# Kernel optimization log

Measured on AMD Instinct MI355X. Metric: run time of the kernel, lower is better.

The kernel has to match this reference:

```python
import jax, jax.numpy as jnp
import numpy as np

B, S, E, H = 2, 2048, 1024, 16
D = E // H  # head_dim = 64


def setup_inputs() -> dict:
    key = jax.random.key(0)
    ks = jax.random.split(key, 6)
    sc = 1.0 / np.sqrt(D)
    return {
        "x": jax.random.normal(ks[0], (B, S, E), dtype=jnp.float32),
        "Wq": jax.random.normal(ks[1], (D, D), dtype=jnp.float32) * sc,
        "Wk": jax.random.normal(ks[2], (D, D), dtype=jnp.float32) * sc,
        "Wv": jax.random.normal(ks[3], (D, D), dtype=jnp.float32) * sc,
        "Wo": jax.random.normal(ks[4], (E, E), dtype=jnp.float32) * (1.0 / np.sqrt(E)),
        "bo": jnp.zeros((E,), dtype=jnp.float32),
    }


def reference(x, Wq, Wk, Wv, Wo, bo):
    b, s, e = x.shape
    # split into heads: (B, H, S, D)
    xh = x.reshape(b, s, H, D).transpose(0, 2, 1, 3)
    # per-head linear projections (weights SHARED across heads); torch Linear: x @ W^T
    q = jnp.einsum('bhsd,ed->bhse', xh, Wq)
    k = jnp.einsum('bhsd,ed->bhse', xh, Wk)
    v = jnp.einsum('bhsd,ed->bhse', xh, Wv)
    # full attention matrix (B, H, S, S) — faithful to the naive original
    energy = jnp.einsum('bhqd,bhkd->bhqk', q, k)
    attn = jax.nn.softmax(energy / jnp.sqrt(jnp.asarray(D, x.dtype)), axis=-1)
    out = jnp.einsum('bhqk,bhkd->bhqd', attn, v)
    out = out.transpose(0, 2, 1, 3).reshape(b, s, e)
    return out @ Wo.T + bo
```

## Files before the change

kernel.cpp:

```cpp
#include <hip/hip_runtime.h>
#include <hip/hip_bf16.h>

#define B 2
#define S 2048
#define E 1024
#define H 16
#define D 64

typedef unsigned short ushort_t;
typedef __attribute__((ext_vector_type(8))) short bf16x8;
typedef __attribute__((ext_vector_type(4))) float f32x4;
typedef __attribute__((ext_vector_type(16))) float f32x16;

static __device__ __forceinline__ ushort_t f2bf(float f) {
    union { float f; unsigned u; } v; v.f = f;
    unsigned r = v.u + 0x7fffu + ((v.u >> 16) & 1u);
    return (ushort_t)(r >> 16);
}

#define MFMA(a, b, c)   __builtin_amdgcn_mfma_f32_16x16x32_bf16((a), (b), (c), 0, 0, 0)
#define MFMA32(a, b, c) __builtin_amdgcn_mfma_f32_32x32x16_bf16((a), (b), (c), 0, 0, 0)
#define PACKBF(hi, lo) __builtin_amdgcn_perm((hi), (lo), 0x07060302u)

__global__ __launch_bounds__(256) void cvt_w(
    const float* __restrict__ Wq, const float* __restrict__ Wk, const float* __restrict__ Wv,
    const float* __restrict__ Wo,
    ushort_t* __restrict__ wqb, ushort_t* __restrict__ wkb, ushort_t* __restrict__ wvb,
    ushort_t* __restrict__ wob)
{
    int gid = blockIdx.x, t = threadIdx.x;
    if (gid < 1024) {
        int i = gid * 1024 + t * 4;
        float4 f = *(const float4*)(Wo + i);
        ushort4 u; u.x = f2bf(f.x); u.y = f2bf(f.y); u.z = f2bf(f.z); u.w = f2bf(f.w);
        *(ushort4*)(wob + i) = u;
    } else {
        int idx = (gid - 1024) * 1024 + t * 4;
        int which = idx >> 12, off = idx & 4095;
        const float* src = (which == 0) ? Wq : (which == 1) ? Wk : Wv;
        ushort_t* dst    = (which == 0) ? wqb : (which == 1) ? wkb : wvb;
        float sc = (which == 0) ? 0.18033688011112042f : 1.0f;
        float4 f = *(const float4*)(src + off);
        ushort4 u; u.x = f2bf(f.x * sc); u.y = f2bf(f.y * sc);
        u.z = f2bf(f.z * sc); u.w = f2bf(f.w * sc);
        *(ushort4*)(dst + off) = u;
    }
}

__global__ __launch_bounds__(256) void qkv_proj(
    const float* __restrict__ x,
    const ushort_t* __restrict__ wq, const ushort_t* __restrict__ wk, const ushort_t* __restrict__ wv,
    ushort_t* __restrict__ q, ushort_t* __restrict__ k, ushort_t* __restrict__ vT)
{
    __shared__ ushort_t Xs[64][72];
    __shared__ ushort_t Wqs[64][72], Wks[64][72], Wvs[64][72];
    int t = threadIdx.x;
    int bh = blockIdx.y, b = bh >> 4, h = bh & 15;
    int s0 = blockIdx.x * 64;

    {
        int i = t >> 2, d0 = (t & 3) * 16;
        const float* xp = x + ((size_t)(b * S + s0 + i)) * E + h * D + d0;
        #pragma unroll
        for (int c = 0; c < 16; c += 4) {
            float4 f = *(const float4*)(xp + c);
            Xs[i][d0 + c + 0] = f2bf(f.x); Xs[i][d0 + c + 1] = f2bf(f.y);
            Xs[i][d0 + c + 2] = f2bf(f.z); Xs[i][d0 + c + 3] = f2bf(f.w);
        }
    }
    {
        int e = t >> 2, d0 = (t & 3) * 16;
        *(bf16x8*)&Wqs[e][d0]     = *(const bf16x8*)(wq + e * 64 + d0);
        *(bf16x8*)&Wqs[e][d0 + 8] = *(const bf16x8*)(wq + e * 64 + d0 + 8);
        *(bf16x8*)&Wks[e][d0]     = *(const bf16x8*)(wk + e * 64 + d0);
        *(bf16x8*)&Wks[e][d0 + 8] = *(const bf16x8*)(wk + e * 64 + d0 + 8);
        *(bf16x8*)&Wvs[e][d0]     = *(const bf16x8*)(wv + e * 64 + d0);
        *(bf16x8*)&Wvs[e][d0 + 8] = *(const bf16x8*)(wv + e * 64 + d0 + 8);
    }
    __syncthreads();

    int w = t >> 6, lane = t & 63, m = lane & 15, quad = lane >> 4;
    bf16x8 a0 = *(bf16x8*)&Xs[16 * w + m][quad * 8];
    bf16x8 a1 = *(bf16x8*)&Xs[16 * w + m][32 + quad * 8];
    f32x4 cq[4], ck[4], cv[4];
    #pragma unroll
    for (int nt = 0; nt < 4; nt++) { cq[nt] = (f32x4)0.f; ck[nt] = (f32x4)0.f; cv[nt] = (f32x4)0.f; }
    #pragma unroll
    for (int nt = 0; nt < 4; nt++) {
        bf16x8 b0, b1;
        b0 = *(bf16x8*)&Wqs[nt * 16 + m][quad * 8]; b1 = *(bf16x8*)&Wqs[nt * 16 + m][32 + quad * 8];
        cq[nt] = MFMA(a0, b0, cq[nt]); cq[nt] = MFMA(a1, b1, cq[nt]);
        b0 = *(bf16x8*)&Wks[nt * 16 + m][quad * 8]; b1 = *(bf16x8*)&Wks[nt * 16 + m][32 + quad * 8];
        ck[nt] = MFMA(a0, b0, ck[nt]); ck[nt] = MFMA(a1, b1, ck[nt]);
        b0 = *(bf16x8*)&Wvs[nt * 16 + m][quad * 8]; b1 = *(bf16x8*)&Wvs[nt * 16 + m][32 + quad * 8];
        cv[nt] = MFMA(a0, b0, cv[nt]); cv[nt] = MFMA(a1, b1, cv[nt]);
    }
    size_t base = (size_t)bh * S + s0;
    #pragma unroll
    for (int nt = 0; nt < 4; nt++)
        #pragma unroll
        for (int r = 0; r < 4; r++) {
            size_t idx = (base + 16 * w + quad * 4 + r) * D + nt * 16 + m;
            q[idx] = f2bf(cq[nt][r]);
            k[idx] = f2bf(ck[nt][r]);
        }
    __syncthreads();
    #pragma unroll
    for (int nt = 0; nt < 4; nt++)
        #pragma unroll
        for (int r = 0; r < 4; r++)
            Wvs[nt * 16 + m][16 * w + quad * 4 + r] = f2bf(cv[nt][r]);
    __syncthreads();
    {
        int d0 = t >> 2, sc = (t & 3) * 16;
        ushort_t* vp = vT + ((size_t)bh * D + d0) * S + s0 + sc;
        *(bf16x8*)(vp)     = *(bf16x8*)&Wvs[d0][sc];
        *(bf16x8*)(vp + 8) = *(bf16x8*)&Wvs[d0][sc + 8];
    }
}

__global__ __launch_bounds__(512, 4) void flash_attn(
    const ushort_t* __restrict__ q, const ushort_t* __restrict__ k,
    const ushort_t* __restrict__ vT, ushort_t* __restrict__ ao)
{
    __shared__ ushort_t Ks[2][2][64][72];
    __shared__ ushort_t Vt[2][2][64][72];
    int t = threadIdx.x;
    int bh = blockIdx.y, b = bh >> 4, h = bh & 15;
    int q0 = blockIdx.x * 128;
    int w = t >> 6, lane = t & 63, l31 = lane & 31, half = lane >> 5;
    int g = w >> 2, wq = w & 3;
    int tg = t & 255;

    const ushort_t* qb = q + ((size_t)bh * S + q0) * D;
    const ushort_t* kb = k + (size_t)bh * S * D;
    const ushort_t* vb = vT + (size_t)bh * D * S;

    bf16x8 qf[4];
    {
        const ushort_t* qp = qb + (size_t)(wq * 32 + l31) * D + half * 8;
        #pragma unroll
        for (int c = 0; c < 4; c++) qf[c] = *(const bf16x8*)(qp + c * 16);
    }

    f32x16 o0 = (f32x16)0.f, o1 = (f32x16)0.f;
    float2 ls2 = make_float2(0.f, 0.f);

    int sr = tg >> 2, scc = (tg & 3) * 16;
    bf16x8 kp0, kp1, vp0, vp1;

    {
        int k00 = g * 64;
        const ushort_t* kp = kb + (size_t)(k00 + sr) * D + scc;
        const ushort_t* vp = vb + (size_t)sr * S + k00 + scc;
        kp0 = *(const bf16x8*)(kp);     kp1 = *(const bf16x8*)(kp + 8);
        vp0 = *(const bf16x8*)(vp);     vp1 = *(const bf16x8*)(vp + 8);
        *(bf16x8*)&Ks[g][0][sr][scc]     = kp0;
        *(bf16x8*)&Ks[g][0][sr][scc + 8] = kp1;
        *(bf16x8*)&Vt[g][0][sr][scc]     = vp0;
        *(bf16x8*)&Vt[g][0][sr][scc + 8] = vp1;
    }
    __syncthreads();
    {
        int k01 = (2 + g) * 64;
        const ushort_t* kp = kb + (size_t)(k01 + sr) * D + scc;
        const ushort_t* vp = vb + (size_t)sr * S + k01 + scc;
        kp0 = *(const bf16x8*)(kp);     kp1 = *(const bf16x8*)(kp + 8);
        vp0 = *(const bf16x8*)(vp);     vp1 = *(const bf16x8*)(vp + 8);
    }

    const int NJ = S / 128;
    for (int jt = 0; jt < NJ; jt++) {
        int p = jt & 1;
        if (jt + 1 < NJ) {
            *(bf16x8*)&Ks[g][1 - p][sr][scc]     = kp0;
            *(bf16x8*)&Ks[g][1 - p][sr][scc + 8] = kp1;
            *(bf16x8*)&Vt[g][1 - p][sr][scc]     = vp0;
            *(bf16x8*)&Vt[g][1 - p][sr][scc + 8] = vp1;
        }
        if (jt + 2 < NJ) {
            int k0n = (2 * (jt + 2) + g) * 64;
            const ushort_t* kp = kb + (size_t)(k0n + sr) * D + scc;
            const ushort_t* vp = vb + (size_t)sr * S + k0n + scc;
            kp0 = *(const bf16x8*)(kp);     kp1 = *(const bf16x8*)(kp + 8);
            vp0 = *(const bf16x8*)(vp);     vp1 = *(const bf16x8*)(vp + 8);
        }

        union { unsigned u[4]; bf16x8 v; } pa[4];
        #pragma unroll
        for (int st = 0; st < 2; st++) {
            f32x16 e = (f32x16)0.f;
            #pragma unroll
            for (int c = 0; c < 4; c++) {
                bf16x8 ka = *(bf16x8*)&Ks[g][p][st * 32 + l31][c * 16 + half * 8];
                e = MFMA32(ka, qf[c], e);
            }
            unsigned pt[16];
            #pragma unroll
            for (int r = 0; r < 16; r += 2) {
                float pe0 = __builtin_amdgcn_exp2f(e[r]);
                float pe1 = __builtin_amdgcn_exp2f(e[r + 1]);
                ls2.x += pe0; ls2.y += pe1;
                pt[r]     = __float_as_uint(pe0);
                pt[r + 1] = __float_as_uint(pe1);
            }
            #pragma unroll
            for (int c2 = 0; c2 < 2; c2++) {
                int rb = c2 * 8;
                unsigned dA = PACKBF(pt[rb + 1], pt[rb + 0]);
                unsigned dB = PACKBF(pt[rb + 3], pt[rb + 2]);
                unsigned dC = PACKBF(pt[rb + 5], pt[rb + 4]);
                unsigned dD = PACKBF(pt[rb + 7], pt[rb + 6]);
                unsigned x1 = (unsigned)__shfl_xor((int)(half ? dA : dC), 32, 64);
                unsigned x2 = (unsigned)__shfl_xor((int)(half ? dB : dD), 32, 64);
                int kc = st * 2 + c2;
                pa[kc].u[0] = half ? x1 : dA;
                pa[kc].u[1] = half ? x2 : dB;
                pa[kc].u[2] = half ? dC : x1;
                pa[kc].u[3] = half ? dD : x2;
            }
        }

        #pragma unroll
        for (int kc = 0; kc < 4; kc++) {
            bf16x8 vf0 = *(bf16x8*)&Vt[g][p][l31][kc * 16 + half * 8];
            bf16x8 vf1 = *(bf16x8*)&Vt[g][p][32 + l31][kc * 16 + half * 8];
            o0 = MFMA32(pa[kc].v, vf0, o0);
            o1 = MFMA32(pa[kc].v, vf1, o1);
        }
        __syncthreads();
    }

    float lsum = ls2.x + ls2.y;
    float* cmb = (float*)&Ks[0][0][0][0];
    int slot = (wq * 64 + lane) * 33;
    if (g == 1) {
        #pragma unroll
        for (int r2 = 0; r2 < 16; r2++) { cmb[slot + r2] = o0[r2]; cmb[slot + 16 + r2] = o1[r2]; }
        cmb[slot + 32] = lsum;
    }
    __syncthreads();
    if (g == 0) {
        #pragma unroll
        for (int r2 = 0; r2 < 16; r2++) { o0[r2] += cmb[slot + r2]; o1[r2] += cmb[slot + 16 + r2]; }
        lsum += cmb[slot + 32];
        float lfull = lsum + __shfl_xor(lsum, 32, 64);
        float inv = 1.001953125f / lfull;
        #pragma unroll
        for (int reg = 0; reg < 16; reg++) {
            int qrow = (reg & 3) + 8 * (reg >> 2) + 4 * half;
            float li = __shfl(inv, qrow, 64);
            int srow = q0 + wq * 32 + qrow;
            size_t base2 = ((size_t)(b * S + srow)) * E + h * D + l31;
            ao[base2]      = f2bf(o0[reg] * li);
            ao[base2 + 32] = f2bf(o1[reg] * li);
        }
    }
}

__global__ __launch_bounds__(256) void out_proj(
    const ushort_t* __restrict__ A, const ushort_t* __restrict__ Wob,
    const float* __restrict__ bo, float* __restrict__ Y)
{
    __shared__ ushort_t As[2][128][72];
    __shared__ ushort_t Ws[2][64][72];
    int t = threadIdx.x;
    int n0 = blockIdx.x * 64, m0 = blockIdx.y * 128;
    int w = t >> 6, lane = t & 63, m = lane & 15, quad = lane >> 4;
    f32x4 acc[2][4];
    #pragma unroll
    for (int u = 0; u < 2; u++)
        #pragma unroll
        for (int nt = 0; nt < 4; nt++) acc[u][nt] = (f32x4)0.f;

    int ar = t >> 1, ac = (t & 1) * 32;
    int wr = t >> 2, wc = (t & 3) * 16;
    const ushort_t* apb = A + (size_t)(m0 + ar) * E + ac;
    const ushort_t* wpb = Wob + (size_t)(n0 + wr) * E + wc;

    bf16x8 arg[4], wrg[2];
    {
        #pragma unroll
        for (int i = 0; i < 4; i++) *(bf16x8*)&As[0][ar][ac + 8 * i] = *(const bf16x8*)(apb + 8 * i);
        *(bf16x8*)&Ws[0][wr][wc]     = *(const bf16x8*)(wpb);
        *(bf16x8*)&Ws[0][wr][wc + 8] = *(const bf16x8*)(wpb + 8);
    }
    __syncthreads();
    {
        #pragma unroll
        for (int i = 0; i < 4; i++) arg[i] = *(const bf16x8*)(apb + 64 + 8 * i);
        wrg[0] = *(const bf16x8*)(wpb + 64);
        wrg[1] = *(const bf16x8*)(wpb + 64 + 8);
    }

    const int KT = E / 64;
    for (int ks = 0; ks < KT; ks++) {
        int p = ks & 1;
        if (ks + 1 < KT) {
            #pragma unroll
            for (int i = 0; i < 4; i++) *(bf16x8*)&As[1 - p][ar][ac + 8 * i] = arg[i];
            *(bf16x8*)&Ws[1 - p][wr][wc]     = wrg[0];
            *(bf16x8*)&Ws[1 - p][wr][wc + 8] = wrg[1];
        }
        if (ks + 2 < KT) {
            int off = (ks + 2) * 64;
            #pragma unroll
            for (int i = 0; i < 4; i++) arg[i] = *(const bf16x8*)(apb + off + 8 * i);
            wrg[0] = *(const bf16x8*)(wpb + off);
            wrg[1] = *(const bf16x8*)(wpb + off + 8);
        }
        #pragma unroll
        for (int h2 = 0; h2 < 2; h2++) {
            bf16x8 af[2];
            af[0] = *(bf16x8*)&As[p][w * 32 + m][h2 * 32 + quad * 8];
            af[1] = *(bf16x8*)&As[p][w * 32 + 16 + m][h2 * 32 + quad * 8];
            #pragma unroll
            for (int nt = 0; nt < 4; nt++) {
                bf16x8 bfr = *(bf16x8*)&Ws[p][nt * 16 + m][h2 * 32 + quad * 8];
                acc[0][nt] = MFMA(af[0], bfr, acc[0][nt]);
                acc[1][nt] = MFMA(af[1], bfr, acc[1][nt]);
            }
        }
        __syncthreads();
    }
    #pragma unroll
    for (int u = 0; u < 2; u++)
        #pragma unroll
        for (int nt = 0; nt < 4; nt++)
            #pragma unroll
            for (int r = 0; r < 4; r++) {
                int row = m0 + w * 32 + u * 16 + quad * 4 + r;
                int col = n0 + nt * 16 + m;
                Y[(size_t)row * E + col] = acc[u][nt][r] + bo[col];
            }
}

extern "C" void kernel_launch(void* const* d_in, const int* in_sizes, int n_in,
                              void* d_out, int out_size, void* d_ws, size_t ws_size,
                              hipStream_t stream)
{
    const float* x  = (const float*)d_in[0];
    const float* Wq = (const float*)d_in[1];
    const float* Wk = (const float*)d_in[2];
    const float* Wv = (const float*)d_in[3];
    const float* Wo = (const float*)d_in[4];
    const float* bo = (const float*)d_in[5];
    float* Y = (float*)d_out;

    const size_t n = (size_t)B * H * S * D;
    ushort_t* qw  = (ushort_t*)d_ws;
    ushort_t* kw  = qw + n;
    ushort_t* vTw = kw + n;
    ushort_t* ao  = vTw + n;
    ushort_t* wob = ao + n;
    ushort_t* wqb = wob + (size_t)E * E;
    ushort_t* wkb = wqb + D * D;
    ushort_t* wvb = wkb + D * D;

    cvt_w<<<dim3(1024 + 12), 256, 0, stream>>>(Wq, Wk, Wv, Wo, wqb, wkb, wvb, wob);
    qkv_proj<<<dim3(S / 64, B * H), 256, 0, stream>>>(x, wqb, wkb, wvb, qw, kw, vTw);
    flash_attn<<<dim3(S / 128, B * H), 512, 0, stream>>>(qw, kw, vTw, ao);
    out_proj<<<dim3(E / 64, (B * S) / 128), 256, 0, stream>>>(ao, wob, bo, Y);
}
```

Baseline: 146.7 us.

## Fuse weight conversion into QKV projection, use permlane32 swap, swizzle out_proj blocks

Removes the separate weight-conversion kernel. The Wo bf16 conversion now runs inside the qkv_proj grid, one 1024-element chunk per block, and each block converts the small Wq/Wk/Wv tiles straight into shared memory. In flash attention the cross-half shuffle plus selects is replaced with v_permlane32_swap_b32 inline asm. out_proj block indices are remapped with a swizzle meant to improve L2 reuse. The goal is to save one kernel launch and some shuffle overhead, at the cost of redundant per-block conversion of the small weights.

```diff
diff --git a/kernel.cpp b/kernel.cpp
--- a/kernel.cpp
+++ b/kernel.cpp
@@ -22,35 +22,12 @@
 #define MFMA32(a, b, c) __builtin_amdgcn_mfma_f32_32x32x16_bf16((a), (b), (c), 0, 0, 0)
 #define PACKBF(hi, lo) __builtin_amdgcn_perm((hi), (lo), 0x07060302u)
 
-__global__ __launch_bounds__(256) void cvt_w(
+__global__ __launch_bounds__(256) void qkv_proj(
+    const float* __restrict__ x,
     const float* __restrict__ Wq, const float* __restrict__ Wk, const float* __restrict__ Wv,
     const float* __restrict__ Wo,
-    ushort_t* __restrict__ wqb, ushort_t* __restrict__ wkb, ushort_t* __restrict__ wvb,
+    ushort_t* __restrict__ q, ushort_t* __restrict__ k, ushort_t* __restrict__ vT,
     ushort_t* __restrict__ wob)
-{
-    int gid = blockIdx.x, t = threadIdx.x;
-    if (gid < 1024) {
-        int i = gid * 1024 + t * 4;
-        float4 f = *(const float4*)(Wo + i);
-        ushort4 u; u.x = f2bf(f.x); u.y = f2bf(f.y); u.z = f2bf(f.z); u.w = f2bf(f.w);
-        *(ushort4*)(wob + i) = u;
-    } else {
-        int idx = (gid - 1024) * 1024 + t * 4;
-        int which = idx >> 12, off = idx & 4095;
-        const float* src = (which == 0) ? Wq : (which == 1) ? Wk : Wv;
-        ushort_t* dst    = (which == 0) ? wqb : (which == 1) ? wkb : wvb;
-        float sc = (which == 0) ? 0.18033688011112042f : 1.0f;
-        float4 f = *(const float4*)(src + off);
-        ushort4 u; u.x = f2bf(f.x * sc); u.y = f2bf(f.y * sc);
-        u.z = f2bf(f.z * sc); u.w = f2bf(f.w * sc);
-        *(ushort4*)(dst + off) = u;
-    }
-}
-
-__global__ __launch_bounds__(256) void qkv_proj(
-    const float* __restrict__ x,
-    const ushort_t* __restrict__ wq, const ushort_t* __restrict__ wk, const ushort_t* __restrict__ wv,
-    ushort_t* __restrict__ q, ushort_t* __restrict__ k, ushort_t* __restrict__ vT)
 {
     __shared__ ushort_t Xs[64][72];
     __shared__ ushort_t Wqs[64][72], Wks[64][72], Wvs[64][72];
@@ -59,6 +36,13 @@
     int s0 = blockIdx.x * 64;
 
     {
+        int woid = blockIdx.y * 32 + blockIdx.x;
+        int i = woid * 1024 + t * 4;
+        float4 f = *(const float4*)(Wo + i);
+        ushort4 u2; u2.x = f2bf(f.x); u2.y = f2bf(f.y); u2.z = f2bf(f.z); u2.w = f2bf(f.w);
+        *(ushort4*)(wob + i) = u2;
+    }
+    {
         int i = t >> 2, d0 = (t & 3) * 16;
         const float* xp = x + ((size_t)(b * S + s0 + i)) * E + h * D + d0;
         #pragma unroll
@@ -70,12 +54,23 @@
     }
     {
         int e = t >> 2, d0 = (t & 3) * 16;
-        *(bf16x8*)&Wqs[e][d0]     = *(const bf16x8*)(wq + e * 64 + d0);
-        *(bf16x8*)&Wqs[e][d0 + 8] = *(const bf16x8*)(wq + e * 64 + d0 + 8);
-        *(bf16x8*)&Wks[e][d0]     = *(const bf16x8*)(wk + e * 64 + d0);
-        *(bf16x8*)&Wks[e][d0 + 8] = *(const bf16x8*)(wk + e * 64 + d0 + 8);
-        *(bf16x8*)&Wvs[e][d0]     = *(const bf16x8*)(wv + e * 64 + d0);
-        *(bf16x8*)&Wvs[e][d0 + 8] = *(const bf16x8*)(wv + e * 64 + d0 + 8);
+        const float* wqp = Wq + e * 64 + d0;
+        const float* wkp = Wk + e * 64 + d0;
+        const float* wvp = Wv + e * 64 + d0;
+        #pragma unroll
+        for (int c = 0; c < 16; c += 4) {
+            float4 fq = *(const float4*)(wqp + c);
+            Wqs[e][d0 + c + 0] = f2bf(fq.x * 0.18033688011112042f);
+            Wqs[e][d0 + c + 1] = f2bf(fq.y * 0.18033688011112042f);
+            Wqs[e][d0 + c + 2] = f2bf(fq.z * 0.18033688011112042f);
+            Wqs[e][d0 + c + 3] = f2bf(fq.w * 0.18033688011112042f);
+            float4 fk = *(const float4*)(wkp + c);
+            Wks[e][d0 + c + 0] = f2bf(fk.x); Wks[e][d0 + c + 1] = f2bf(fk.y);
+            Wks[e][d0 + c + 2] = f2bf(fk.z); Wks[e][d0 + c + 3] = f2bf(fk.w);
+            float4 fv = *(const float4*)(wvp + c);
+            Wvs[e][d0 + c + 0] = f2bf(fv.x); Wvs[e][d0 + c + 1] = f2bf(fv.y);
+            Wvs[e][d0 + c + 2] = f2bf(fv.z); Wvs[e][d0 + c + 3] = f2bf(fv.w);
+        }
     }
     __syncthreads();
 
@@ -211,13 +206,13 @@
                 unsigned dB = PACKBF(pt[rb + 3], pt[rb + 2]);
                 unsigned dC = PACKBF(pt[rb + 5], pt[rb + 4]);
                 unsigned dD = PACKBF(pt[rb + 7], pt[rb + 6]);
-                unsigned x1 = (unsigned)__shfl_xor((int)(half ? dA : dC), 32, 64);
-                unsigned x2 = (unsigned)__shfl_xor((int)(half ? dB : dD), 32, 64);
+                asm volatile("v_permlane32_swap_b32 %0, %1" : "+v"(dA), "+v"(dC));
+                asm volatile("v_permlane32_swap_b32 %0, %1" : "+v"(dB), "+v"(dD));
                 int kc = st * 2 + c2;
-                pa[kc].u[0] = half ? x1 : dA;
-                pa[kc].u[1] = half ? x2 : dB;
-                pa[kc].u[2] = half ? dC : x1;
-                pa[kc].u[3] = half ? dD : x2;
+                pa[kc].u[0] = dA;
+                pa[kc].u[1] = dB;
+                pa[kc].u[2] = dC;
+                pa[kc].u[3] = dD;
             }
         }
 
@@ -265,7 +260,9 @@
     __shared__ ushort_t As[2][128][72];
     __shared__ ushort_t Ws[2][64][72];
     int t = threadIdx.x;
-    int n0 = blockIdx.x * 64, m0 = blockIdx.y * 128;
+    int hwb = blockIdx.y * 16 + blockIdx.x;
+    int swz = (hwb & 7) * 64 + (hwb >> 3);
+    int n0 = (swz & 15) * 64, m0 = (swz >> 4) * 128;
     int w = t >> 6, lane = t & 63, m = lane & 15, quad = lane >> 4;
     f32x4 acc[2][4];
     #pragma unroll
@@ -353,12 +350,8 @@
     ushort_t* vTw = kw + n;
     ushort_t* ao  = vTw + n;
     ushort_t* wob = ao + n;
-    ushort_t* wqb = wob + (size_t)E * E;
-    ushort_t* wkb = wqb + D * D;
-    ushort_t* wvb = wkb + D * D;
-
-    cvt_w<<<dim3(1024 + 12), 256, 0, stream>>>(Wq, Wk, Wv, Wo, wqb, wkb, wvb, wob);
-    qkv_proj<<<dim3(S / 64, B * H), 256, 0, stream>>>(x, wqb, wkb, wvb, qw, kw, vTw);
+
+    qkv_proj<<<dim3(S / 64, B * H), 256, 0, stream>>>(x, Wq, Wk, Wv, Wo, qw, kw, vTw, wob);
     flash_attn<<<dim3(S / 128, B * H), 512, 0, stream>>>(qw, kw, vTw, ao);
     out_proj<<<dim3(E / 64, (B * S) / 128), 256, 0, stream>>>(ao, wob, bo, Y);
 }
```

Result: no change. 147.9 us (+0.8%).
